# Optimization experiments

Measured on AMD Instinct MI355X. Metric: run time of the kernel, lower is better.

Reference implementation:

```python
import jax, jax.numpy as jnp
import numpy as np

N_NODES = 50000
N_EDGES = 800000
IN_C, HID_C, OUT_C = 128, 128, 64


def gcn_conv(x, src, dst, W, b, n_nodes):
    """PyG GCNConv: add self-loops, symmetric deg^-1/2 normalization,
    linear transform, scatter-add aggregation at target nodes, add bias."""
    # in-degree over (A + I), unit edge weights
    deg = jax.ops.segment_sum(jnp.ones(dst.shape[0], dtype=x.dtype), dst,
                              num_segments=n_nodes)
    dinv = jnp.where(deg > 0, jax.lax.rsqrt(deg), 0.0)
    norm = dinv[src] * dinv[dst]                      # [E+N]
    h = x @ W                                          # [N, out]
    msg = h[src] * norm[:, None]                       # gather + scale
    out = jax.ops.segment_sum(msg, dst, num_segments=n_nodes)  # scatter-add
    return out + b


def setup_inputs() -> dict:
    key = jax.random.key(0)
    k1, k2, k3, k4 = jax.random.split(key, 4)
    x = jax.random.normal(k1, (N_NODES, IN_C), dtype=jnp.float32)
    edge_index = jax.random.randint(k2, (2, N_EDGES), 0, N_NODES, dtype=jnp.int32)
    # Glorot-ish init for weights, zero bias (PyG default bias=True, zeros)
    W1 = jax.random.normal(k3, (IN_C, HID_C), dtype=jnp.float32) * (1.0 / np.sqrt(IN_C))
    b1 = jnp.zeros((HID_C,), dtype=jnp.float32)
    W2 = jax.random.normal(k4, (HID_C, OUT_C), dtype=jnp.float32) * (1.0 / np.sqrt(HID_C))
    b2 = jnp.zeros((OUT_C,), dtype=jnp.float32)
    return {"x": x, "edge_index": edge_index, "W1": W1, "b1": b1, "W2": W2, "b2": b2}


def reference(x, edge_index, W1, b1, W2, b2):
    n_nodes = x.shape[0]
    # add self-loops once (shared by both conv layers)
    loop = jnp.arange(n_nodes, dtype=edge_index.dtype)
    src = jnp.concatenate([edge_index[0], loop])
    dst = jnp.concatenate([edge_index[1], loop])
    h = gcn_conv(x, src, dst, W1, b1, n_nodes)
    h = jax.nn.relu(h)
    out = gcn_conv(h, src, dst, W2, b2, n_nodes)
    return out
```

## Files before the change

kernel.cpp:

```cpp
#include <hip/hip_runtime.h>
#include <hip/hip_fp16.h>


#define N_NODES 50000
#define N_EDGES 800000
#define BINW    128
#define NBIN    391
#define CAP     2560
#define CAP2    6656
#define B_CHUNK 4096
#define NB_SCAT ((N_EDGES + B_CHUNK - 1) / B_CHUNK)

typedef __bf16 bf16x8 __attribute__((ext_vector_type(8)));
typedef float  f32x4  __attribute__((ext_vector_type(4)));

template<int N>
__device__ inline void wprep_body(const float* __restrict__ W,
                                  __bf16* __restrict__ hi, __bf16* __restrict__ lo,
                                  int idx) {
    if (idx >= (N / 16) * 4 * 64) return;
    int l = idx & 63;
    int s = (idx >> 6) & 3;
    int c = idx >> 8;
    int n = c * 16 + (l & 15);
    int k0 = s * 32 + (l >> 4) * 8;
#pragma unroll
    for (int j = 0; j < 8; j++) {
        float w = W[(k0 + j) * N + n];
        __bf16 h = (__bf16)w;
        hi[idx * 8 + j] = h;
        lo[idx * 8 + j] = (__bf16)(w - (float)h);
    }
}

__global__ __launch_bounds__(256) void prep_kernel(
        const float* __restrict__ W1, const float* __restrict__ W2,
        __bf16* __restrict__ w1hi, __bf16* __restrict__ w1lo,
        __bf16* __restrict__ w2hi, __bf16* __restrict__ w2lo,
        int* __restrict__ gcur, __half* __restrict__ hs1, __half* __restrict__ hs2) {
    int b = blockIdx.x, tid = threadIdx.x;
    if (b < 8)       wprep_body<128>(W1, w1hi, w1lo, b * 256 + tid);
    else if (b < 12) wprep_body<64> (W2, w2hi, w2lo, (b - 8) * 256 + tid);
    else {
        for (int i = tid; i < NBIN; i += 256) gcur[i] = 0;
        if (tid < 128) hs1[(size_t)N_NODES * 128 + tid] = __float2half(0.f);
        if (tid < 64)  hs2[(size_t)N_NODES * 64 + tid] = __float2half(0.f);
    }
}


__global__ __launch_bounds__(256) void bin_scatter_kernel(
        const int* __restrict__ src, const int* __restrict__ dst,
        int* __restrict__ gcur, unsigned* __restrict__ ebin) {
    __shared__ int cnt[512];
    __shared__ int boff[512];
    __shared__ int bcur[512];
    __shared__ int gbase[512];
    __shared__ unsigned stage[B_CHUNK];
    __shared__ int ex[256];
    int tid = threadIdx.x;
    int e0 = blockIdx.x * B_CHUNK;

    cnt[tid] = 0; cnt[tid + 256] = 0;
    __syncthreads();

    unsigned key[16]; int bins[16];
#pragma unroll
    for (int i = 0; i < 16; i++) {
        int e = e0 + tid + i * 256;
        if (e < N_EDGES) {
            int d = dst[e], s = src[e];
            key[i]  = ((unsigned)d << 16) | (unsigned)s;
            bins[i] = d >> 7;
            atomicAdd(&cnt[bins[i]], 1);
        } else bins[i] = -1;
    }
    __syncthreads();

    int a = cnt[2 * tid], b = cnt[2 * tid + 1];
    ex[tid] = a + b;
    __syncthreads();
    for (int off = 1; off < 256; off <<= 1) {
        int t = (tid >= off) ? ex[tid - off] : 0;
        __syncthreads();
        ex[tid] += t;
        __syncthreads();
    }
    int myex = ex[tid] - (a + b);
    boff[2 * tid] = myex;     boff[2 * tid + 1] = myex + a;
    bcur[2 * tid] = myex;     bcur[2 * tid + 1] = myex + a;
    __syncthreads();

#pragma unroll
    for (int i = 0; i < 16; i++) {
        if (bins[i] >= 0) {
            int p = atomicAdd(&bcur[bins[i]], 1);
            stage[p] = key[i];
        }
    }

    __syncthreads();
    for (int b2 = tid; b2 < NBIN; b2 += 256) {
        int c = cnt[b2];
        gbase[b2] = (c > 0) ? atomicAdd(&gcur[b2], c) : 0;
    }
    __syncthreads();

    int total = N_EDGES - e0; if (total > B_CHUNK) total = B_CHUNK;
    for (int i = tid; i < total; i += 256) {
        unsigned k = stage[i];
        int bin = (int)(k >> 23);
        int idx = gbase[bin] + (i - boff[bin]);
        if (idx < CAP) ebin[(size_t)bin * CAP + idx] = k;
    }
}

__global__ __launch_bounds__(256) void bin_build_kernel(
        const unsigned* __restrict__ ebin, const int* __restrict__ gcur,
        int* __restrict__ deg, int* __restrict__ row_off,
        float* __restrict__ dinv, int* __restrict__ ssrc) {
    __shared__ int dl[BINW];
    __shared__ int pref[BINW];
    __shared__ int cur[BINW];
    __shared__ int padTotal;
    int bin = blockIdx.x, tid = threadIdx.x;
    if (tid < BINW) dl[tid] = 0;
    __syncthreads();
    int cnt = gcur[bin]; if (cnt > CAP) cnt = CAP;
    const unsigned* eb = ebin + (size_t)bin * CAP;
    for (int i = tid; i < cnt; i += 256)
        atomicAdd(&dl[(eb[i] >> 16) & 127], 1);
    __syncthreads();
    int pc = 0;
    if (tid < BINW) { pc = (dl[tid] + 31) & ~31; pref[tid] = pc; }
    __syncthreads();
    for (int off = 1; off < BINW; off <<= 1) {
        int t = 0;
        if (tid < BINW && tid >= off) t = pref[tid - off];
        __syncthreads();
        if (tid < BINW) pref[tid] += t;
        __syncthreads();
    }
    if (tid < BINW) {
        int ex = pref[tid] - pc;
        cur[tid] = ex;
        int node = bin * BINW + tid;
        if (node < N_NODES) {
            deg[node]     = dl[tid];
            row_off[node] = bin * CAP2 + ex;
            dinv[node]    = rsqrtf((float)(dl[tid] + 1));
        }
        if (tid == BINW - 1) padTotal = pref[tid];
    }
    __syncthreads();
    int pt = padTotal;
    int* sb = ssrc + (size_t)bin * CAP2;
    for (int i = tid; i < pt; i += 256) sb[i] = N_NODES;
    __syncthreads();
    for (int i = tid; i < cnt; i += 256) {
        unsigned k = eb[i];
        int p = atomicAdd(&cur[(k >> 16) & 127], 1);
        sb[p] = (int)(k & 0xFFFFu);
    }
}

template<int OUTC>
__global__ __launch_bounds__(256) void gemm_mfma_kernel(
        const float* __restrict__ X, const __bf16* __restrict__ Whi,
        const __bf16* __restrict__ Wlo, const float* __restrict__ dinv,
        __half* __restrict__ hs) {
    constexpr int NC = OUTC / 16;
    int tid = threadIdx.x;
    int w = tid >> 6, lane = tid & 63;
    int q = lane >> 4, lr = lane & 15;
    int rb = blockIdx.x * 64 + w * 16;
    int row = rb + lr;
    int rowc = (row < N_NODES) ? row : (N_NODES - 1);

    f32x4 acc[NC];
#pragma unroll
    for (int c = 0; c < NC; c++) acc[c] = (f32x4){0.f, 0.f, 0.f, 0.f};

#pragma unroll
    for (int s = 0; s < 4; s++) {
        const float* xp = X + (size_t)rowc * 128 + s * 32 + q * 8;
        float4 x0 = *(const float4*)xp;
        float4 x1 = *(const float4*)(xp + 4);
        float xv[8] = {x0.x, x0.y, x0.z, x0.w, x1.x, x1.y, x1.z, x1.w};
        bf16x8 a_hi, a_lo;
#pragma unroll
        for (int j = 0; j < 8; j++) {
            __bf16 h = (__bf16)xv[j];
            a_hi[j] = h;
            a_lo[j] = (__bf16)(xv[j] - (float)h);
        }
#pragma unroll
        for (int c = 0; c < NC; c++) {
            size_t fo = (size_t)((c * 4 + s) * 64 + lane) * 8;
            bf16x8 bh = *(const bf16x8*)(Whi + fo);
            bf16x8 bl = *(const bf16x8*)(Wlo + fo);
            acc[c] = __builtin_amdgcn_mfma_f32_16x16x32_bf16(a_hi, bh, acc[c], 0, 0, 0);
            acc[c] = __builtin_amdgcn_mfma_f32_16x16x32_bf16(a_lo, bh, acc[c], 0, 0, 0);
            acc[c] = __builtin_amdgcn_mfma_f32_16x16x32_bf16(a_hi, bl, acc[c], 0, 0, 0);
        }
    }

#pragma unroll
    for (int r = 0; r < 4; r++) {
        int grow = rb + q * 4 + r;
        if (grow < N_NODES) {
            float sc = dinv[grow];
#pragma unroll
            for (int c = 0; c < NC; c++) {
                hs[(size_t)grow * OUTC + c * 16 + lr] = __float2half(acc[c][r] * sc);
            }
        }
    }
}

template<bool RELU>
__global__ __launch_bounds__(256) void aggregate128_kernel(
        const __half* __restrict__ hs, const int* __restrict__ row_off,
        const int* __restrict__ deg, const int* __restrict__ ssrc,
        const float* __restrict__ dinv, const float* __restrict__ bias,
        float* __restrict__ out) {
    int node = (blockIdx.x * 256 + threadIdx.x) >> 6;
    int lane = threadIdx.x & 63;
    if (node >= N_NODES) return;
    int beg = row_off[node];
    int d   = deg[node];
    float di = dinv[node];
    int hf = lane >> 5, sl = lane & 31;
    const float2* Hq = (const float2*)hs;
    float4 acc = make_float4(0.f, 0.f, 0.f, 0.f);
    for (int j = 0; j < d; j += 16) {
        int s[8]; float2 v[8];
#pragma unroll
        for (int u = 0; u < 8; u++) s[u] = ssrc[beg + j + 2 * u + hf];
#pragma unroll
        for (int u = 0; u < 8; u++) v[u] = Hq[(size_t)s[u] * 32 + sl];
#pragma unroll
        for (int u = 0; u < 8; u++) {
            float2 f0 = __half22float2(((const __half2*)&v[u])[0]);
            float2 f1 = __half22float2(((const __half2*)&v[u])[1]);
            acc.x += f0.x; acc.y += f0.y; acc.z += f1.x; acc.w += f1.y;
        }
    }
    acc.x += __shfl_xor(acc.x, 32, 64);
    acc.y += __shfl_xor(acc.y, 32, 64);
    acc.z += __shfl_xor(acc.z, 32, 64);
    acc.w += __shfl_xor(acc.w, 32, 64);
    if (hf == 0) {
        float2 sv = Hq[(size_t)node * 32 + sl];
        float2 f0 = __half22float2(((const __half2*)&sv)[0]);
        float2 f1 = __half22float2(((const __half2*)&sv)[1]);
        float4 b = ((const float4*)bias)[sl];
        float4 o;
        o.x = fmaf(di, acc.x + f0.x, b.x);
        o.y = fmaf(di, acc.y + f0.y, b.y);
        o.z = fmaf(di, acc.z + f1.x, b.z);
        o.w = fmaf(di, acc.w + f1.y, b.w);
        if (RELU) {
            o.x = fmaxf(o.x, 0.f); o.y = fmaxf(o.y, 0.f);
            o.z = fmaxf(o.z, 0.f); o.w = fmaxf(o.w, 0.f);
        }
        ((float4*)out)[(size_t)node * 32 + sl] = o;
    }
}

__global__ __launch_bounds__(256) void aggregate64_kernel(
        const __half* __restrict__ hs, const int* __restrict__ row_off,
        const int* __restrict__ deg, const int* __restrict__ ssrc,
        const float* __restrict__ dinv, const float* __restrict__ bias,
        float* __restrict__ out) {
    int node = (blockIdx.x * 256 + threadIdx.x) >> 6;
    int lane = threadIdx.x & 63;
    if (node >= N_NODES) return;
    int beg = row_off[node];
    int d   = deg[node];
    float di = dinv[node];
    int qt = lane >> 4, sl = lane & 15;
    const float2* Hq = (const float2*)hs;
    float4 acc = make_float4(0.f, 0.f, 0.f, 0.f);
    for (int j = 0; j < d; j += 32) {
        int s[8]; float2 v[8];
#pragma unroll
        for (int u = 0; u < 8; u++) s[u] = ssrc[beg + j + 4 * u + qt];
#pragma unroll
        for (int u = 0; u < 8; u++) v[u] = Hq[(size_t)s[u] * 16 + sl];
#pragma unroll
        for (int u = 0; u < 8; u++) {
            float2 f0 = __half22float2(((const __half2*)&v[u])[0]);
            float2 f1 = __half22float2(((const __half2*)&v[u])[1]);
            acc.x += f0.x; acc.y += f0.y; acc.z += f1.x; acc.w += f1.y;
        }
    }
    acc.x += __shfl_xor(acc.x, 16, 64);
    acc.y += __shfl_xor(acc.y, 16, 64);
    acc.z += __shfl_xor(acc.z, 16, 64);
    acc.w += __shfl_xor(acc.w, 16, 64);
    acc.x += __shfl_xor(acc.x, 32, 64);
    acc.y += __shfl_xor(acc.y, 32, 64);
    acc.z += __shfl_xor(acc.z, 32, 64);
    acc.w += __shfl_xor(acc.w, 32, 64);
    if (lane < 16) {
        float2 sv = Hq[(size_t)node * 16 + sl];
        float2 f0 = __half22float2(((const __half2*)&sv)[0]);
        float2 f1 = __half22float2(((const __half2*)&sv)[1]);
        float4 b = ((const float4*)bias)[sl];
        float4 o;
        o.x = fmaf(di, acc.x + f0.x, b.x);
        o.y = fmaf(di, acc.y + f0.y, b.y);
        o.z = fmaf(di, acc.z + f1.x, b.z);
        o.w = fmaf(di, acc.w + f1.y, b.w);
        ((float4*)out)[(size_t)node * 16 + sl] = o;
    }
}


extern "C" void kernel_launch(void* const* d_in, const int* in_sizes, int n_in,
                              void* d_out, int out_size, void* d_ws, size_t ws_size,
                              hipStream_t stream) {
    const float* x  = (const float*)d_in[0];
    const int*   ei = (const int*)d_in[1];
    const float* W1 = (const float*)d_in[2];
    const float* b1 = (const float*)d_in[3];
    const float* W2 = (const float*)d_in[4];
    const float* b2 = (const float*)d_in[5];
    float* out = (float*)d_out;

    const int* src = ei;
    const int* dst = ei + N_EDGES;

    char* p = (char*)d_ws;
    size_t off = 0;
    auto alloc = [&](size_t bytes) { void* q = p + off; off += (bytes + 255) & ~(size_t)255; return q; };
    float*    dinv    = (float*)   alloc(N_NODES * 4);
    int*      deg     = (int*)     alloc(N_NODES * 4);
    int*      row_off = (int*)     alloc(N_NODES * 4);
    int*      gcur    = (int*)     alloc(NBIN * 4);
    int*      ssrc    = (int*)     alloc((size_t)NBIN * CAP2 * 4);
    unsigned* ebin    = (unsigned*)alloc((size_t)NBIN * CAP * 4);
    __bf16*   w1hi    = (__bf16*)  alloc(128 * 128 * 2);
    __bf16*   w1lo    = (__bf16*)  alloc(128 * 128 * 2);
    __bf16*   w2hi    = (__bf16*)  alloc(128 * 64 * 2);
    __bf16*   w2lo    = (__bf16*)  alloc(128 * 64 * 2);
    __half*   hs1     = (__half*)  alloc((size_t)(N_NODES + 1) * 128 * 2);
    __half*   hs2     = (__half*)  alloc((size_t)(N_NODES + 1) * 64 * 2);
    float*    x2      = (float*)   alloc((size_t)N_NODES * 128 * 4);

    prep_kernel<<<13, 256, 0, stream>>>(W1, W2, w1hi, w1lo, w2hi, w2lo, gcur, hs1, hs2);
    bin_scatter_kernel<<<NB_SCAT, 256, 0, stream>>>(src, dst, gcur, ebin);
    bin_build_kernel<<<NBIN, 256, 0, stream>>>(ebin, gcur, deg, row_off, dinv, ssrc);

    gemm_mfma_kernel<128><<<(N_NODES + 63) / 64, 256, 0, stream>>>(x, w1hi, w1lo, dinv, hs1);
    aggregate128_kernel<true><<<(N_NODES * 64 + 255) / 256, 256, 0, stream>>>(
        hs1, row_off, deg, ssrc, dinv, b1, x2);

    gemm_mfma_kernel<64><<<(N_NODES + 63) / 64, 256, 0, stream>>>(x2, w2hi, w2lo, dinv, hs2);
    aggregate64_kernel<<<(N_NODES * 64 + 255) / 256, 256, 0, stream>>>(
        hs2, row_off, deg, ssrc, dinv, b2, out);
}
```

Baseline: 184.9 us.

## Fuse layer-1 aggregation with layer-2 GEMM via shared memory; halve scatter chunk

Layer-1 aggregation (with bias and ReLU) now writes each 16-node tile into shared memory, and the same 1024-thread block runs the layer-2 MFMA GEMM on it, producing the scaled fp16 hs2 directly. This removes the fp32 x2 intermediate (a 25.6MB write plus reread) and one kernel launch. In exchange, only 4 of the 16 waves do the GEMM after a block-wide barrier, which may lower occupancy. Separately, the bin-scatter chunk is halved to 2048 edges, doubling the number of blocks and the global bin atomics.

```diff
diff --git a/kernel.cpp b/kernel.cpp
--- a/kernel.cpp
+++ b/kernel.cpp
@@ -8,7 +8,7 @@
 #define NBIN    391
 #define CAP     2560
 #define CAP2    6656
-#define B_CHUNK 4096
+#define B_CHUNK 2048
 #define NB_SCAT ((N_EDGES + B_CHUNK - 1) / B_CHUNK)
 
 typedef __bf16 bf16x8 __attribute__((ext_vector_type(8)));
@@ -64,9 +64,9 @@
     cnt[tid] = 0; cnt[tid + 256] = 0;
     __syncthreads();
 
-    unsigned key[16]; int bins[16];
-#pragma unroll
-    for (int i = 0; i < 16; i++) {
+    unsigned key[8]; int bins[8];
+#pragma unroll
+    for (int i = 0; i < 8; i++) {
         int e = e0 + tid + i * 256;
         if (e < N_EDGES) {
             int d = dst[e], s = src[e];
@@ -92,7 +92,7 @@
     __syncthreads();
 
 #pragma unroll
-    for (int i = 0; i < 16; i++) {
+    for (int i = 0; i < 8; i++) {
         if (bins[i] >= 0) {
             int p = atomicAdd(&bcur[bins[i]], 1);
             stage[p] = key[i];
@@ -164,12 +164,11 @@
     }
 }
 
-template<int OUTC>
-__global__ __launch_bounds__(256) void gemm_mfma_kernel(
+__global__ __launch_bounds__(256) void gemm_mfma128_kernel(
         const float* __restrict__ X, const __bf16* __restrict__ Whi,
         const __bf16* __restrict__ Wlo, const float* __restrict__ dinv,
         __half* __restrict__ hs) {
-    constexpr int NC = OUTC / 16;
+    constexpr int NC = 8;
     int tid = threadIdx.x;
     int w = tid >> 6, lane = tid & 63;
     int q = lane >> 4, lr = lane & 15;
@@ -212,26 +211,29 @@
             float sc = dinv[grow];
 #pragma unroll
             for (int c = 0; c < NC; c++) {
-                hs[(size_t)grow * OUTC + c * 16 + lr] = __float2half(acc[c][r] * sc);
+                hs[(size_t)grow * 128 + c * 16 + lr] = __float2half(acc[c][r] * sc);
             }
         }
     }
 }
 
-template<bool RELU>
-__global__ __launch_bounds__(256) void aggregate128_kernel(
-        const __half* __restrict__ hs, const int* __restrict__ row_off,
+__global__ __launch_bounds__(1024) void fused_agg_gemm_kernel(
+        const __half* __restrict__ hs1, const int* __restrict__ row_off,
         const int* __restrict__ deg, const int* __restrict__ ssrc,
         const float* __restrict__ dinv, const float* __restrict__ bias,
-        float* __restrict__ out) {
-    int node = (blockIdx.x * 256 + threadIdx.x) >> 6;
+        const __bf16* __restrict__ w2hi, const __bf16* __restrict__ w2lo,
+        __half* __restrict__ hs2) {
+    __shared__ float x2buf[16][132];
+    int wave = threadIdx.x >> 6;
     int lane = threadIdx.x & 63;
-    if (node >= N_NODES) return;
+    int rb = blockIdx.x * 16;
+    int node = rb + wave;
+
     int beg = row_off[node];
     int d   = deg[node];
     float di = dinv[node];
     int hf = lane >> 5, sl = lane & 31;
-    const float2* Hq = (const float2*)hs;
+    const float2* Hq = (const float2*)hs1;
     float4 acc = make_float4(0.f, 0.f, 0.f, 0.f);
     for (int j = 0; j < d; j += 16) {
         int s[8]; float2 v[8];
@@ -256,15 +258,43 @@
         float2 f1 = __half22float2(((const __half2*)&sv)[1]);
         float4 b = ((const float4*)bias)[sl];
         float4 o;
-        o.x = fmaf(di, acc.x + f0.x, b.x);
-        o.y = fmaf(di, acc.y + f0.y, b.y);
-        o.z = fmaf(di, acc.z + f1.x, b.z);
-        o.w = fmaf(di, acc.w + f1.y, b.w);
-        if (RELU) {
-            o.x = fmaxf(o.x, 0.f); o.y = fmaxf(o.y, 0.f);
-            o.z = fmaxf(o.z, 0.f); o.w = fmaxf(o.w, 0.f);
-        }
-        ((float4*)out)[(size_t)node * 32 + sl] = o;
+        o.x = fmaxf(fmaf(di, acc.x + f0.x, b.x), 0.f);
+        o.y = fmaxf(fmaf(di, acc.y + f0.y, b.y), 0.f);
+        o.z = fmaxf(fmaf(di, acc.z + f1.x, b.z), 0.f);
+        o.w = fmaxf(fmaf(di, acc.w + f1.y, b.w), 0.f);
+        *(float4*)&x2buf[wave][4 * sl] = o;
+    }
+    __syncthreads();
+
+    if (threadIdx.x < 256) {
+        int c = wave;
+        int q = lane >> 4, lr = lane & 15;
+        f32x4 g = (f32x4){0.f, 0.f, 0.f, 0.f};
+#pragma unroll
+        for (int s = 0; s < 4; s++) {
+            const float* xp = &x2buf[lr][s * 32 + q * 8];
+            float4 a0 = *(const float4*)xp;
+            float4 a1 = *(const float4*)(xp + 4);
+            float xv[8] = {a0.x, a0.y, a0.z, a0.w, a1.x, a1.y, a1.z, a1.w};
+            bf16x8 a_hi, a_lo;
+#pragma unroll
+            for (int j = 0; j < 8; j++) {
+                __bf16 h = (__bf16)xv[j];
+                a_hi[j] = h;
+                a_lo[j] = (__bf16)(xv[j] - (float)h);
+            }
+            size_t fo = (size_t)((c * 4 + s) * 64 + lane) * 8;
+            bf16x8 bh = *(const bf16x8*)(w2hi + fo);
+            bf16x8 bl = *(const bf16x8*)(w2lo + fo);
+            g = __builtin_amdgcn_mfma_f32_16x16x32_bf16(a_hi, bh, g, 0, 0, 0);
+            g = __builtin_amdgcn_mfma_f32_16x16x32_bf16(a_lo, bh, g, 0, 0, 0);
+            g = __builtin_amdgcn_mfma_f32_16x16x32_bf16(a_hi, bl, g, 0, 0, 0);
+        }
+#pragma unroll
+        for (int r = 0; r < 4; r++) {
+            int grow = rb + q * 4 + r;
+            hs2[(size_t)grow * 64 + c * 16 + lr] = __float2half(g[r] * dinv[grow]);
+        }
     }
 }
 
@@ -347,17 +377,14 @@
     __bf16*   w2lo    = (__bf16*)  alloc(128 * 64 * 2);
     __half*   hs1     = (__half*)  alloc((size_t)(N_NODES + 1) * 128 * 2);
     __half*   hs2     = (__half*)  alloc((size_t)(N_NODES + 1) * 64 * 2);
-    float*    x2      = (float*)   alloc((size_t)N_NODES * 128 * 4);
 
     prep_kernel<<<13, 256, 0, stream>>>(W1, W2, w1hi, w1lo, w2hi, w2lo, gcur, hs1, hs2);
     bin_scatter_kernel<<<NB_SCAT, 256, 0, stream>>>(src, dst, gcur, ebin);
     bin_build_kernel<<<NBIN, 256, 0, stream>>>(ebin, gcur, deg, row_off, dinv, ssrc);
 
-    gemm_mfma_kernel<128><<<(N_NODES + 63) / 64, 256, 0, stream>>>(x, w1hi, w1lo, dinv, hs1);
-    aggregate128_kernel<true><<<(N_NODES * 64 + 255) / 256, 256, 0, stream>>>(
-        hs1, row_off, deg, ssrc, dinv, b1, x2);
-
-    gemm_mfma_kernel<64><<<(N_NODES + 63) / 64, 256, 0, stream>>>(x2, w2hi, w2lo, dinv, hs2);
+    gemm_mfma128_kernel<<<(N_NODES + 63) / 64, 256, 0, stream>>>(x, w1hi, w1lo, dinv, hs1);
+    fused_agg_gemm_kernel<<<N_NODES / 16, 1024, 0, stream>>>(
+        hs1, row_off, deg, ssrc, dinv, b1, w2hi, w2lo, hs2);
     aggregate64_kernel<<<(N_NODES * 64 + 255) / 256, 256, 0, stream>>>(
         hs2, row_off, deg, ssrc, dinv, b2, out);
 }
```

New measurement: 184.8 us. No clear change (-0.1%).
